# Optimization experiments

Hardware: AMD Instinct MI355X
Metric: run time of the kernel (lower is better)

Reference implementation:

```python
import jax, jax.numpy as jnp
import numpy as np

# 5G NR LDPC BG1-like parameters
Z = 384          # lifting factor
MB, NB = 46, 68  # basegraph rows / cols (BG1)
DEG = 7          # check-node base degree (~316/46 edges of real BG1)
K = 8448         # info bits (= k_ldpc = 22*Z, no filler bits)
N = 25344        # transmitted bits = n_ldpc - 2*Z (rate 1/3)
N_LDPC = NB * Z  # 26112 variable nodes
M = MB * Z       # 17664 check nodes
E = MB * DEG * Z # 123648 edges
NUM_ITER = 20
LLR_MAX = 20.0
BATCH = 128


def _build_graph():
    """Deterministic lifted quasi-cyclic Tanner graph (BG1-like)."""
    rng = np.random.default_rng(0)
    rows, cols = [], []
    i = np.arange(Z)
    for r in range(MB):
        cs = rng.choice(NB, DEG, replace=False)
        for c in cs:
            shift = int(rng.integers(Z))
            rows.append(r * Z + i)
            cols.append(c * Z + (i + shift) % Z)
    return (np.concatenate(rows).astype(np.int32),
            np.concatenate(cols).astype(np.int32))


def setup_inputs() -> dict:
    key = jax.random.key(0)
    row, col = _build_graph()
    llr_ch = 4.0 * jax.random.normal(key, (BATCH, N), dtype=jnp.float32)
    return {"llr_ch": llr_ch, "row": jnp.asarray(row), "col": jnp.asarray(col)}


def _decode(llr_ch, row, col):
    """5G rate recovery + flooding min-sum BP, soft info-bit LLR output."""
    B = llr_ch.shape[0]
    llr = jnp.clip(llr_ch, -LLR_MAX, LLR_MAX)
    # de-rate-matching: first 2*Z systematic bits are punctured -> LLR 0
    llr_full = jnp.concatenate([jnp.zeros((B, 2 * Z), llr.dtype), llr], axis=1)
    # Sionna LLR convention log p(1)/p(0): negate for internal BP
    lch = -llr_full.T                       # [N_LDPC, B]
    eid = jnp.arange(E)
    inf = jnp.asarray(1e9, lch.dtype)
    m_cv0 = jnp.zeros((E, B), lch.dtype)

    def step(m_cv, _):
        # ---- VN update (extrinsic) ----
        vn_sum = lch + jax.ops.segment_sum(m_cv, col, num_segments=N_LDPC)
        m_vc = vn_sum[col] - m_cv           # [E, B]
        # ---- CN update: min-sum with exclude-self min ----
        mag = jnp.abs(m_vc)
        neg = m_vc < 0
        min1 = jax.ops.segment_min(mag, row, num_segments=M)       # [M, B]
        is_min = mag <= min1[row]
        cand = jnp.where(is_min, eid[:, None], E)
        first = jax.ops.segment_min(cand, row, num_segments=M)     # first argmin
        is_the_min = eid[:, None] == first[row]
        min2 = jax.ops.segment_min(jnp.where(is_the_min, inf, mag),
                                   row, num_segments=M)
        out_mag = jnp.where(is_the_min, min2[row], min1[row])
        n_neg = jax.ops.segment_sum(neg.astype(jnp.int32), row, num_segments=M)
        sign_tot = (1 - 2 * (n_neg % 2))[row].astype(mag.dtype)
        sign_excl = sign_tot * jnp.where(neg, -1.0, 1.0)           # s_tot / s_e
        return sign_excl * out_mag, None

    m_cv, _ = jax.lax.scan(step, m_cv0, None, length=NUM_ITER)
    x_tot = lch + jax.ops.segment_sum(m_cv, col, num_segments=N_LDPC)
    llr_out = -x_tot.T                      # back to p(1)/p(0) convention
    return llr_out[:, :K]                   # systematic info-bit LLRs


def reference(llr_ch, row, col):
    return _decode(llr_ch, row, col)
```

## Files before the change

### kernel.cpp

```cpp
#include <hip/hip_runtime.h>

#define Zl      384
#define MBr     46
#define NBc     68
#define DEG     7
#define K_INFO  8448
#define N_TX    25344
#define N_LDPC  (NBc * Zl)
#define M_CHK   (MBr * Zl)
#define E_EDGE  (MBr * DEG * Zl)
#define BATCH   128
#define NUM_ITER 20
#define LLR_MAXF 20.0f
#define BCAP    32

#define NPG      69
#define NBLK     (NPG * 8)
#define CN_TILES (M_CHK / 128)
#define VN_TILES (N_LDPC / 128)



__global__ void prep_kernel(const float* __restrict__ llr, float* __restrict__ lch) {
    __shared__ float tile[32][33];
    const int n0 = blockIdx.x * 32, b0 = blockIdx.y * 32;
    const int tx = threadIdx.x, ty = threadIdx.y;
#pragma unroll
    for (int j = 0; j < 4; ++j) {
        float v = llr[(b0 + ty + 8 * j) * N_TX + n0 + tx];
        v = fminf(fmaxf(v, -LLR_MAXF), LLR_MAXF);
        tile[ty + 8 * j][tx] = -v;
    }
    __syncthreads();
#pragma unroll
    for (int j = 0; j < 4; ++j) {
        const int b = b0 + tx;
        const int n = n0 + ty + 8 * j;
        lch[((size_t)(b >> 3) * N_LDPC + 2 * Zl + n) * 8 + (b & 7)] = tile[tx][ty + 8 * j];
    }
}

__global__ void base_build_kernel(const int* __restrict__ col,
                                  int* __restrict__ bcount, int* __restrict__ badj,
                                  int* __restrict__ cadj) {
    __shared__ int sc[MBr * DEG];
    __shared__ int ssh[MBr * DEG];
    const int t = threadIdx.x;
    if (t < MBr * DEG) {
        const int v0 = col[t * Zl];
        const int c  = v0 / Zl;
        sc[t]  = c;
        ssh[t] = v0 - c * Zl;
        cadj[t] = ssh[t] | (sc[t] << 10);
    }
    if (t < NBc) bcount[t] = 0;
    __syncthreads();
    if (t < MBr * DEG) {
        const int c = sc[t];
        int slot = 0;
        for (int u = 0; u < t; ++u) slot += (sc[u] == c) ? 1 : 0;
        const int r = t / DEG, d = t - r * DEG;
        if (slot < BCAP) badj[c * BCAP + slot] = ssh[t] | (d << 10) | (r << 13);
        atomicAdd(&bcount[c], 1);
    }
}

__device__ __forceinline__ void gsync(unsigned* cnt, unsigned* gen) {
    __syncthreads();
    if (threadIdx.x == 0) {
        const unsigned g0 = __hip_atomic_load(gen, __ATOMIC_RELAXED, __HIP_MEMORY_SCOPE_AGENT);
        const unsigned old = __hip_atomic_fetch_add(cnt, 1u, __ATOMIC_RELAXED, __HIP_MEMORY_SCOPE_AGENT);
        if (old == (unsigned)(NPG - 1)) {
            __hip_atomic_store(cnt, 0u, __ATOMIC_RELAXED, __HIP_MEMORY_SCOPE_AGENT);
            asm volatile("s_waitcnt vmcnt(0)" ::: "memory");
            __hip_atomic_store(gen, g0 + 1u, __ATOMIC_RELAXED, __HIP_MEMORY_SCOPE_AGENT);
        } else {
            while (__hip_atomic_load(gen, __ATOMIC_RELAXED, __HIP_MEMORY_SCOPE_AGENT) == g0)
                __builtin_amdgcn_s_sleep(2);
        }
        asm volatile("buffer_inv sc0\n\ts_waitcnt vmcnt(0)" ::: "memory");
    }
    __syncthreads();
}

template <bool FIRST>
__device__ __forceinline__ void cn_tile(const float* __restrict__ xin,
                                        float* __restrict__ state_f2,
                                        unsigned short* __restrict__ meta,
                                        const int* __restrict__ cadj,
                                        const int s, const int cn, const int ql) {
    const int r = cn / Zl;
    const int i = cn - r * Zl;

    const float4* xp = (const float4*)xin + (size_t)s * N_LDPC * 2;
    float4* sp = (float4*)state_f2 + ((size_t)s * M_CHK + cn) * 4 + ql * 2;
    ushort4* mp = (ushort4*)meta + ((size_t)s * M_CHK + cn) * 2 + ql;

    float omin1[4], omin2[4];
    int oamin[4]; unsigned onm[4], ostot[4];
    if (!FIRST) {
        const float4 sA = sp[0];
        const float4 sB = sp[1];
        omin1[0] = sA.x; omin2[0] = sA.y; omin1[1] = sA.z; omin2[1] = sA.w;
        omin1[2] = sB.x; omin2[2] = sB.y; omin1[3] = sB.z; omin2[3] = sB.w;
        const ushort4 mt = mp[0];
        const unsigned m4[4] = {mt.x, mt.y, mt.z, mt.w};
#pragma unroll
        for (int c = 0; c < 4; ++c) {
            oamin[c] = m4[c] & 7u;
            onm[c]   = (m4[c] >> 3) & 0x7Fu;
            ostot[c] = (m4[c] >> 10) & 1u;
        }
    }

    float min1[4] = {1e30f, 1e30f, 1e30f, 1e30f};
    float min2[4] = {1e30f, 1e30f, 1e30f, 1e30f};
    int   amin[4] = {0, 0, 0, 0};
    unsigned nm[4] = {0u, 0u, 0u, 0u};

#pragma unroll
    for (int d = 0; d < DEG; ++d) {
        const int pk = cadj[r * DEG + d];
        const int sh = pk & 0x3FF;
        const int c  = pk >> 10;
        int ii = i + sh; if (ii >= Zl) ii -= Zl;
        const int v = c * Zl + ii;
        const float4 xv = xp[(size_t)v * 2 + ql];
        float t[4] = {xv.x, xv.y, xv.z, xv.w};
        if (!FIRST) {
#pragma unroll
            for (int c2 = 0; c2 < 4; ++c2) {
                const float omag = (d == oamin[c2]) ? omin2[c2] : omin1[c2];
                const float mold = (ostot[c2] ^ ((onm[c2] >> d) & 1u)) ? -omag : omag;
                t[c2] -= mold;
            }
        }
#pragma unroll
        for (int c2 = 0; c2 < 4; ++c2) {
            const float mag = fabsf(t[c2]);
            nm[c2] |= (t[c2] < 0.f ? 1u : 0u) << d;
            if (mag < min1[c2]) { min2[c2] = min1[c2]; min1[c2] = mag; amin[c2] = d; }
            else if (mag < min2[c2]) { min2[c2] = mag; }
        }
    }

    float4 oA, oB;
    oA.x = min1[0]; oA.y = min2[0]; oA.z = min1[1]; oA.w = min2[1];
    oB.x = min1[2]; oB.y = min2[2]; oB.z = min1[3]; oB.w = min2[3];
    sp[0] = oA;
    sp[1] = oB;
    ushort4 mo;
    unsigned mv[4];
#pragma unroll
    for (int c = 0; c < 4; ++c)
        mv[c] = (unsigned)amin[c] | (nm[c] << 3) | ((unsigned)(__popc(nm[c]) & 1) << 10);
    mo.x = (unsigned short)mv[0]; mo.y = (unsigned short)mv[1];
    mo.z = (unsigned short)mv[2]; mo.w = (unsigned short)mv[3];
    mp[0] = mo;
}

__device__ __forceinline__ void vn_tile(const float* __restrict__ lch,
                                        const float* __restrict__ state_f2,
                                        const unsigned short* __restrict__ meta,
                                        const int* __restrict__ bcount,
                                        const int* __restrict__ badj,
                                        float* __restrict__ x,
                                        const int s, const int v, const int ql) {
    const int c = v / Zl;
    const int j = v - c * Zl;
    const int cnt = min(bcount[c], BCAP);
    const int* bp = badj + c * BCAP;
    const float4* stp = (const float4*)state_f2 + (size_t)s * M_CHK * 4;
    const ushort4* mtp = (const ushort4*)meta + (size_t)s * M_CHK * 2;

    float4 sacc = ((const float4*)lch)[((size_t)s * N_LDPC + v) * 2 + ql];
    for (int k = 0; k < cnt; ++k) {
        const int pk = bp[k];
        const int sh = pk & 0x3FF;
        const int d  = (pk >> 10) & 7;
        const int r  = pk >> 13;
        int i = j - sh;
        if (i < 0) i += Zl;
        const int cnb = r * Zl + i;
        const float4 sA = stp[(size_t)cnb * 4 + ql * 2];
        const float4 sB = stp[(size_t)cnb * 4 + ql * 2 + 1];
        const ushort4 mt = mtp[(size_t)cnb * 2 + ql];
        const unsigned m4[4] = {mt.x, mt.y, mt.z, mt.w};
        const float mn1[4] = {sA.x, sA.z, sB.x, sB.z};
        const float mn2[4] = {sA.y, sA.w, sB.y, sB.w};
        float val[4];
#pragma unroll
        for (int cc = 0; cc < 4; ++cc) {
            const int   am  = m4[cc] & 7u;
            const unsigned nmv = (m4[cc] >> 3) & 0x7Fu;
            const unsigned st  = (m4[cc] >> 10) & 1u;
            const float mag = (d == am) ? mn2[cc] : mn1[cc];
            val[cc] = (st ^ ((nmv >> d) & 1u)) ? -mag : mag;
        }
        sacc.x += val[0]; sacc.y += val[1]; sacc.z += val[2]; sacc.w += val[3];
    }
    ((float4*)x)[((size_t)s * N_LDPC + v) * 2 + ql] = sacc;
}

__global__ void __launch_bounds__(256, 4)
decode_persist(const float* __restrict__ lch, float* __restrict__ x,
               float* __restrict__ state, unsigned short* __restrict__ meta,
               const int* __restrict__ bcount, const int* __restrict__ badj,
               const int* __restrict__ cadj, unsigned* __restrict__ bar) {
    const int g  = blockIdx.x & 7;
    const int bg = blockIdx.x >> 3;
    const int nl = threadIdx.x >> 1;
    const int ql = threadIdx.x & 1;
    unsigned* cnt = bar + (size_t)g * 64;
    unsigned* gen = bar + (size_t)g * 64 + 32;

    for (int h = 0; h < 2; ++h) {
        const int s = h * 8 + g;
        for (int t = 0; t < NUM_ITER; ++t) {
            if (t == 0) {
                cn_tile<true>(lch, state, meta, cadj, s, bg * 128 + nl, ql);
                cn_tile<true>(lch, state, meta, cadj, s, (bg + NPG) * 128 + nl, ql);
            } else {
                cn_tile<false>(x, state, meta, cadj, s, bg * 128 + nl, ql);
                cn_tile<false>(x, state, meta, cadj, s, (bg + NPG) * 128 + nl, ql);
            }
            gsync(cnt, gen);
            for (int tile = bg; tile < VN_TILES; tile += NPG)
                vn_tile(lch, state, meta, bcount, badj, x, s, tile * 128 + nl, ql);
            if (t != NUM_ITER - 1) gsync(cnt, gen);
        }
    }
}

__global__ void out_kernel(const float* __restrict__ x, float* __restrict__ out) {
    __shared__ float tile[32][33];
    const int k0 = blockIdx.x * 32, b0 = blockIdx.y * 32;
    const int tx = threadIdx.x, ty = threadIdx.y;
#pragma unroll
    for (int j = 0; j < 4; ++j) {
        const int b = b0 + tx;
        const int k = k0 + ty + 8 * j;
        tile[ty + 8 * j][tx] = -x[((size_t)(b >> 3) * N_LDPC + k) * 8 + (b & 7)];
    }
    __syncthreads();
#pragma unroll
    for (int j = 0; j < 4; ++j) {
        out[(b0 + ty + 8 * j) * K_INFO + k0 + tx] = tile[tx][ty + 8 * j];
    }
}

extern "C" void kernel_launch(void* const* d_in, const int* in_sizes, int n_in,
                              void* d_out, int out_size, void* d_ws, size_t ws_size,
                              hipStream_t stream) {
    const float* llr = (const float*)d_in[0];
    const int* col = (const int*)d_in[2];
    float* out = (float*)d_out;

    char* ws = (char*)d_ws;
    float* lch   = (float*)ws;
    float* x     = lch + (size_t)N_LDPC * BATCH;
    float* state = x + (size_t)N_LDPC * BATCH;
    unsigned short* meta = (unsigned short*)(state + (size_t)M_CHK * BATCH * 2);
    int* bcount = (int*)(meta + (size_t)M_CHK * BATCH);
    int* badj   = bcount + NBc;
    int* cadj   = badj + NBc * BCAP;
    size_t bar_off = (size_t)((char*)(cadj + 512) - ws);
    bar_off = (bar_off + 511) & ~(size_t)511;
    unsigned* bar = (unsigned*)(ws + bar_off);

    hipMemsetAsync(lch, 0, (size_t)N_LDPC * BATCH * sizeof(float), stream);
    hipMemsetAsync(bar, 0, 8 * 64 * sizeof(unsigned), stream);

    prep_kernel<<<dim3(N_TX / 32, BATCH / 32), dim3(32, 8), 0, stream>>>(llr, lch);
    base_build_kernel<<<1, 512, 0, stream>>>(col, bcount, badj, cadj);

    decode_persist<<<NBLK, 256, 0, stream>>>(lch, x, state, meta,
                                             bcount, badj, cadj, bar);

    out_kernel<<<dim3(K_INFO / 32, BATCH / 32), dim3(32, 8), 0, stream>>>(x, out);
}
```

Baseline: 853.3 us.

## Rebalance persistent decode with cost-weighted VN partitioning and monotonic barrier

Raises the number of persistent blocks per group from 69 to 96 (768 total), splits check-node work into contiguous per-block unit ranges, and partitions variable-node work with a prefix sum weighted by each column's degree, computed in the setup kernel. The grid barrier becomes a single monotonically increasing counter compared against a per-phase target, replacing the count-reset-plus-generation scheme. The aim is to even out per-block work, since VN degrees vary by column, and to shorten barrier latency. In exchange, more co-resident blocks must fit for the spin barrier to be safe, and the contiguous VN ranges change the memory access pattern.

```diff
diff --git a/kernel.cpp b/kernel.cpp
--- a/kernel.cpp
+++ b/kernel.cpp
@@ -14,10 +14,12 @@
 #define LLR_MAXF 20.0f
 #define BCAP    32
 
-#define NPG      69
+#define NPG      96
 #define NBLK     (NPG * 8)
-#define CN_TILES (M_CHK / 128)
-#define VN_TILES (N_LDPC / 128)
+#define CN_UNITS (M_CHK * 2)
+#define CN_PER_BLK (CN_UNITS / NPG)
+#define CN_TAIL  (CN_PER_BLK - 256)
+#define VN_UNITS (N_LDPC * 2)
 
 
 
@@ -42,7 +44,7 @@
 
 __global__ void base_build_kernel(const int* __restrict__ col,
                                   int* __restrict__ bcount, int* __restrict__ badj,
-                                  int* __restrict__ cadj) {
+                                  int* __restrict__ cadj, int* __restrict__ vb) {
     __shared__ int sc[MBr * DEG];
     __shared__ int ssh[MBr * DEG];
     const int t = threadIdx.x;
@@ -63,28 +65,49 @@
         if (slot < BCAP) badj[c * BCAP + slot] = ssh[t] | (d << 10) | (r << 13);
         atomicAdd(&bcount[c], 1);
     }
-}
-
-__device__ __forceinline__ void gsync(unsigned* cnt, unsigned* gen) {
+    __syncthreads();
+    if (t == 0) {
+        long long colpref[NBc + 1];
+        colpref[0] = 0;
+        for (int c = 0; c < NBc; ++c) {
+            const int cost = min(bcount[c], BCAP) + 2;
+            colpref[c + 1] = colpref[c] + (long long)cost * (2 * Zl);
+        }
+        const long long total = colpref[NBc];
+        vb[0] = 0;
+        int c = 0, prev = 0;
+        for (int k = 1; k < NPG; ++k) {
+            const long long target = (total * k) / NPG;
+            while (colpref[c + 1] <= target) ++c;
+            const int cost = min(bcount[c], BCAP) + 2;
+            long long u = (long long)c * (2 * Zl) + (target - colpref[c]) / cost;
+            int ui = (int)(u & ~63LL);
+            if (ui < prev) ui = prev;
+            vb[k] = ui;
+            prev = ui;
+        }
+        vb[NPG] = VN_UNITS;
+    }
+}
+
+__device__ __forceinline__ void gsync(unsigned* cnt, unsigned target) {
     __syncthreads();
     if (threadIdx.x == 0) {
-        const unsigned g0 = __hip_atomic_load(gen, __ATOMIC_RELAXED, __HIP_MEMORY_SCOPE_AGENT);
-        const unsigned old = __hip_atomic_fetch_add(cnt, 1u, __ATOMIC_RELAXED, __HIP_MEMORY_SCOPE_AGENT);
-        if (old == (unsigned)(NPG - 1)) {
-            __hip_atomic_store(cnt, 0u, __ATOMIC_RELAXED, __HIP_MEMORY_SCOPE_AGENT);
-            asm volatile("s_waitcnt vmcnt(0)" ::: "memory");
-            __hip_atomic_store(gen, g0 + 1u, __ATOMIC_RELAXED, __HIP_MEMORY_SCOPE_AGENT);
-        } else {
-            while (__hip_atomic_load(gen, __ATOMIC_RELAXED, __HIP_MEMORY_SCOPE_AGENT) == g0)
+        const unsigned old = __hip_atomic_fetch_add(cnt, 1u, __ATOMIC_RELAXED,
+                                                    __HIP_MEMORY_SCOPE_AGENT);
+        if (old + 1u != target) {
+            while (__hip_atomic_load(cnt, __ATOMIC_RELAXED,
+                                     __HIP_MEMORY_SCOPE_AGENT) < target)
                 __builtin_amdgcn_s_sleep(2);
         }
-        asm volatile("buffer_inv sc0\n\ts_waitcnt vmcnt(0)" ::: "memory");
+        asm volatile("buffer_inv sc0\n\t"
+                     "s_waitcnt vmcnt(0)" ::: "memory");
     }
     __syncthreads();
 }
 
 template <bool FIRST>
-__device__ __forceinline__ void cn_tile(const float* __restrict__ xin,
+__device__ __forceinline__ void cn_unit(const float* __restrict__ xin,
                                         float* __restrict__ state_f2,
                                         unsigned short* __restrict__ meta,
                                         const int* __restrict__ cadj,
@@ -159,7 +182,7 @@
     mp[0] = mo;
 }
 
-__device__ __forceinline__ void vn_tile(const float* __restrict__ lch,
+__device__ __forceinline__ void vn_unit(const float* __restrict__ lch,
                                         const float* __restrict__ state_f2,
                                         const unsigned short* __restrict__ meta,
                                         const int* __restrict__ bcount,
@@ -206,28 +229,38 @@
 decode_persist(const float* __restrict__ lch, float* __restrict__ x,
                float* __restrict__ state, unsigned short* __restrict__ meta,
                const int* __restrict__ bcount, const int* __restrict__ badj,
-               const int* __restrict__ cadj, unsigned* __restrict__ bar) {
+               const int* __restrict__ cadj, const int* __restrict__ vb,
+               unsigned* __restrict__ bar) {
     const int g  = blockIdx.x & 7;
     const int bg = blockIdx.x >> 3;
-    const int nl = threadIdx.x >> 1;
-    const int ql = threadIdx.x & 1;
     unsigned* cnt = bar + (size_t)g * 64;
-    unsigned* gen = bar + (size_t)g * 64 + 32;
+    const int vu0 = vb[bg], vu1 = vb[bg + 1];
+    const int cu0 = bg * CN_PER_BLK;
+    unsigned nb = 0;
 
     for (int h = 0; h < 2; ++h) {
         const int s = h * 8 + g;
         for (int t = 0; t < NUM_ITER; ++t) {
-            if (t == 0) {
-                cn_tile<true>(lch, state, meta, cadj, s, bg * 128 + nl, ql);
-                cn_tile<true>(lch, state, meta, cadj, s, (bg + NPG) * 128 + nl, ql);
-            } else {
-                cn_tile<false>(x, state, meta, cadj, s, bg * 128 + nl, ql);
-                cn_tile<false>(x, state, meta, cadj, s, (bg + NPG) * 128 + nl, ql);
+            {
+                const int u = cu0 + threadIdx.x;
+                if (t == 0) {
+                    cn_unit<true>(lch, state, meta, cadj, s, u >> 1, u & 1);
+                    if (threadIdx.x < CN_TAIL) {
+                        const int u2 = u + 256;
+                        cn_unit<true>(lch, state, meta, cadj, s, u2 >> 1, u2 & 1);
+                    }
+                } else {
+                    cn_unit<false>(x, state, meta, cadj, s, u >> 1, u & 1);
+                    if (threadIdx.x < CN_TAIL) {
+                        const int u2 = u + 256;
+                        cn_unit<false>(x, state, meta, cadj, s, u2 >> 1, u2 & 1);
+                    }
+                }
             }
-            gsync(cnt, gen);
-            for (int tile = bg; tile < VN_TILES; tile += NPG)
-                vn_tile(lch, state, meta, bcount, badj, x, s, tile * 128 + nl, ql);
-            if (t != NUM_ITER - 1) gsync(cnt, gen);
+            ++nb; gsync(cnt, nb * NPG);
+            for (int u = vu0 + threadIdx.x; u < vu1; u += 256)
+                vn_unit(lch, state, meta, bcount, badj, x, s, u >> 1, u & 1);
+            if (t != NUM_ITER - 1) { ++nb; gsync(cnt, nb * NPG); }
         }
     }
 }
@@ -264,7 +297,8 @@
     int* bcount = (int*)(meta + (size_t)M_CHK * BATCH);
     int* badj   = bcount + NBc;
     int* cadj   = badj + NBc * BCAP;
-    size_t bar_off = (size_t)((char*)(cadj + 512) - ws);
+    int* vb     = cadj + MBr * DEG;
+    size_t bar_off = (size_t)((char*)(vb + NPG + 1) - ws);
     bar_off = (bar_off + 511) & ~(size_t)511;
     unsigned* bar = (unsigned*)(ws + bar_off);
 
@@ -272,10 +306,10 @@
     hipMemsetAsync(bar, 0, 8 * 64 * sizeof(unsigned), stream);
 
     prep_kernel<<<dim3(N_TX / 32, BATCH / 32), dim3(32, 8), 0, stream>>>(llr, lch);
-    base_build_kernel<<<1, 512, 0, stream>>>(col, bcount, badj, cadj);
+    base_build_kernel<<<1, 512, 0, stream>>>(col, bcount, badj, cadj, vb);
 
     decode_persist<<<NBLK, 256, 0, stream>>>(lch, x, state, meta,
-                                             bcount, badj, cadj, bar);
+                                             bcount, badj, cadj, vb, bar);
 
     out_kernel<<<dim3(K_INFO / 32, BATCH / 32), dim3(32, 8), 0, stream>>>(x, out);
 }
```

Result: slower. 1.616 ms (+89.4%).
